# Kernel optimization log

Hardware: AMD Instinct MI355X
Metric: run time of the kernel (lower is better)

The kernel has to match this reference:

```python
import jax, jax.numpy as jnp
import numpy as np

B, S, V, D, H, L = 256, 512, 32000, 100, 75, 128

def setup_inputs() -> dict:
    key = jax.random.key(0)
    ks = jax.random.split(key, 10)
    def lin(k, out_f, in_f):
        bound = 1.0 / np.sqrt(in_f)
        kw, kb = jax.random.split(k)
        W = jax.random.uniform(kw, (out_f, in_f), jnp.float32, -bound, bound)
        b = jax.random.uniform(kb, (out_f,), jnp.float32, -bound, bound)
        return W, b
    W1, b1 = lin(ks[0], H, D)   # i2h_fc1
    W2, b2 = lin(ks[1], H, H)   # i2h_fc2
    Wo, bo = lin(ks[2], H, H)   # h2o_fc
    Wfc, bfc = lin(ks[3], L, H) # fc
    emb = jax.random.normal(ks[4], (V, D), jnp.float32)
    X = jax.random.randint(ks[5], (B, S), 0, V)
    return {"X": X, "emb": emb, "W1": W1, "b1": b1, "W2": W2, "b2": b2,
            "Wo": Wo, "bo": bo, "Wfc": Wfc, "bfc": bfc}

def reference(X, emb, W1, b1, W2, b2, Wo, bo, Wfc, bfc):
    x = emb[X]                                   # [B,S,D] embedding lookup (dropout off: is_training=False)
    xp = jnp.einsum('bsd,hd->bsh', x, W1) + b1   # precompute input projection for all steps
    h0 = jnp.zeros((X.shape[0], W2.shape[0]), x.dtype)

    def step(h, xp_t):
        h = jax.nn.sigmoid(xp_t + h @ W2.T + b2)       # Elman hidden update
        o = jax.nn.sigmoid(h @ Wo.T + bo)              # per-step output
        return h, o

    _, outs = jax.lax.scan(step, h0, jnp.swapaxes(xp, 0, 1))  # [S,B,H]
    outs = jnp.swapaxes(outs, 0, 1)                            # [B,S,H] (batch_first)
    return jnp.einsum('bsh,lh->bsl', outs, Wfc) + bfc          # [B,S,L]
```

## Files before the change

kernel.cpp:

```cpp
#include <hip/hip_runtime.h>
#include <hip/hip_bf16.h>

typedef unsigned int uint;
typedef unsigned short ushort;

constexpr int Bn = 256, Sn = 512, Vn = 32000, Dn = 100, Hn = 75, Ln = 128;
constexpr int EW = 80;
constexpr int KP = 96;
constexpr int W2S = 80;

constexpr size_t OFF_EMBW = 0;
constexpr size_t OFF_HALL = OFF_EMBW + (size_t)Vn*EW;
constexpr size_t OFF_W2P  = OFF_HALL + (size_t)Bn*Sn*KP/2;
constexpr size_t OFF_WOH  = OFF_W2P + 3200;
constexpr size_t OFF_WFH  = OFF_WOH + 3840;

typedef __attribute__((ext_vector_type(2))) _Float16 half2_t;
typedef __attribute__((ext_vector_type(8))) _Float16 half8;
typedef __attribute__((ext_vector_type(4))) float floatx4;

__device__ __forceinline__ ushort f2h(float f){
    union { _Float16 h; ushort u; } v; v.h = (_Float16)f; return v.u;
}
__device__ __forceinline__ half8 as_h8(uint4 u){
    union { uint4 u; half8 h; } v; v.u = u; return v.h;
}
__device__ __forceinline__ float sigmoidf(float z){
    return __builtin_amdgcn_rcpf(1.f + __expf(-z));
}

__global__ __launch_bounds__(256) void k_wprep(
    const float* __restrict__ W2, const float* __restrict__ Wo,
    const float* __restrict__ Wfc, ushort* __restrict__ w2p,
    ushort* __restrict__ woh, ushort* __restrict__ wfh, ushort* __restrict__ h_all)
{
    const int tid = blockIdx.x*256 + threadIdx.x;
    const int stride = gridDim.x*256;
    for (int i = tid; i < 80*W2S; i += stride){
        int r = i / W2S, k = i % W2S;
        w2p[i] = (r < Hn && k < Hn) ? f2h(W2[r*Hn + k]) : (ushort)0;
    }
    for (int i = tid; i < 80*KP; i += stride){
        int r = i / KP, k = i % KP;
        woh[i] = (r < Hn && k < Hn) ? f2h(Wo[r*Hn + k]) : (ushort)0;
    }
    for (int i = tid; i < Ln*KP; i += stride){
        int l = i / KP, k = i % KP;
        wfh[i] = (k < Hn) ? f2h(Wfc[l*Hn + k]) : (ushort)0;
    }
    uint* hu = (uint*)h_all;
    for (int i = tid; i < Bn*Sn*8; i += stride){
        int row = i >> 3, c = i & 7;
        hu[(size_t)row*48 + 40 + c] = 0u;
    }
}

__global__ __attribute__((amdgpu_flat_work_group_size(256,256)))
__attribute__((amdgpu_waves_per_eu(1,1)))
void k_embproj(
    const float* __restrict__ emb, const float* __restrict__ W1,
    const float* __restrict__ b1, const float* __restrict__ b2,
    float* __restrict__ embW)
{
    const int lane = threadIdx.x & 63;
    const int w    = threadIdx.x >> 6;
    const int v = blockIdx.x*64 + lane;
    const float4* ev = (const float4*)(emb + (size_t)v*Dn);
    float e[Dn];
    #pragma unroll
    for (int q = 0; q < Dn/4; ++q){
        float4 x = ev[q];
        e[4*q] = x.x; e[4*q+1] = x.y; e[4*q+2] = x.z; e[4*q+3] = x.w;
    }
    __shared__ float s_out[64*EW];
    const int j0 = w*19;
    const int jend = (w == 3) ? 18 : 19;
    #pragma unroll 2
    for (int jj = 0; jj < jend; ++jj){
        int j = j0 + jj;
        float a0 = b1[j] + b2[j], a1 = 0.f, a2 = 0.f, a3 = 0.f;
        const float* wp = W1 + j*Dn;
        #pragma unroll
        for (int d = 0; d < Dn; d += 4){
            a0 += wp[d]*e[d];     a1 += wp[d+1]*e[d+1];
            a2 += wp[d+2]*e[d+2]; a3 += wp[d+3]*e[d+3];
        }
        s_out[lane*EW + j] = (a0+a1) + (a2+a3);
    }
    if (w == 3){
        #pragma unroll
        for (int j = Hn; j < EW; ++j) s_out[lane*EW + j] = 0.f;
    }
    __syncthreads();
    float* dst = embW + (size_t)blockIdx.x*64*EW;
    for (int i = threadIdx.x; i < 64*EW; i += 256) dst[i] = s_out[i];
}

__global__ __attribute__((amdgpu_flat_work_group_size(256,256)))
__attribute__((amdgpu_waves_per_eu(1,1)))
void k_rnn(
    const int* __restrict__ X, const float* __restrict__ embW,
    const ushort* __restrict__ w2p, ushort* __restrict__ h_all,
    const ushort* __restrict__ woh, const ushort* __restrict__ wfh,
    const float* __restrict__ bo, const float* __restrict__ bfc,
    float* __restrict__ out)
{
    const int b   = blockIdx.x;
    const int tid = threadIdx.x;
    const int L   = tid & 63;
    const int wv  = tid >> 6;
    const int m   = L & 15;
    const int g   = L >> 4;
    __shared__ int sX[Sn];
    __shared__ __align__(16) float xpb[2][64*80];
    __shared__ __align__(16) ushort o_lds[4][16*104];

    for (int i = tid; i < Sn; i += 256) sX[i] = X[b*Sn + i];

    half8 bfr[5][3];
    if (wv == 0){
        #pragma unroll
        for (int t = 0; t < 5; ++t){
            #pragma unroll
            for (int ks = 0; ks < 3; ++ks){
                int k0 = ks*32 + g*8;
                half8 bv = {};
                if (k0 < 80) bv = *(const half8*)(w2p + (size_t)(16*t + m)*W2S + k0);
                bfr[t][ks] = bv;
            }
        }
    }
    __syncthreads();

    auto stage = [&](int c){
        float* buf = xpb[c & 1];
        const int base = c*64;
        #pragma unroll
        for (int k = 0; k < 5; ++k){
            int idx = k*256 + tid;
            int cs  = idx / 20;
            int off = idx - cs*20;
            int tok = sX[base + cs];
            const float* src = embW + (size_t)tok*EW + off*4;
            __builtin_amdgcn_global_load_lds(
                (const __attribute__((address_space(1))) uint*)src,
                (__attribute__((address_space(3))) uint*)(buf + idx*4),
                16, 0, 0);
        }
    };

    int va0 = 32*g,      va1 = 32*g + 8,  va2 = 32*g + 16, va3 = 32*g + 24;
    int vb0 = va0 + 128, vb1 = va1 + 128, vb2 = va2 + 128, vb3 = va3 + 128;

    ushort* hout = h_all + (size_t)b*Sn*KP;
    const floatx4 zero4 = {};
    uint4 A0 = {}, A1 = {}, A2 = {};

    stage(0);
    for (int c = 0; c < 8; ++c){
        __syncthreads();
        if (c < 7) stage(c + 1);
        if (wv == 0){
            const float* xp = xpb[c & 1];
            float x1c = xp[L];
            float x2c = (L < 16) ? xp[64 + L] : 0.f;
            float x1n = xp[80 + L];
            float x2n = (L < 16) ? xp[80 + 64 + L] : 0.f;
            for (int t = 0; t < 64; ++t){
                int pf = (t + 2 < 64) ? t + 2 : 63;
                float x1f = xp[pf*80 + L];
                float x2f = (L < 16) ? xp[pf*80 + 64 + L] : 0.f;

                half8 af0 = as_h8(A0), af1 = as_h8(A1), af2 = as_h8(A2);

                floatx4 acc0, acc1, acc2, acc3, acc4;
                acc0 = __builtin_amdgcn_mfma_f32_16x16x32_f16(af0, bfr[0][0], zero4, 0,0,0);
                acc1 = __builtin_amdgcn_mfma_f32_16x16x32_f16(af0, bfr[1][0], zero4, 0,0,0);
                acc2 = __builtin_amdgcn_mfma_f32_16x16x32_f16(af0, bfr[2][0], zero4, 0,0,0);
                acc3 = __builtin_amdgcn_mfma_f32_16x16x32_f16(af0, bfr[3][0], zero4, 0,0,0);
                acc4 = __builtin_amdgcn_mfma_f32_16x16x32_f16(af0, bfr[4][0], zero4, 0,0,0);
                acc0 = __builtin_amdgcn_mfma_f32_16x16x32_f16(af1, bfr[0][1], acc0, 0,0,0);
                acc1 = __builtin_amdgcn_mfma_f32_16x16x32_f16(af1, bfr[1][1], acc1, 0,0,0);
                acc2 = __builtin_amdgcn_mfma_f32_16x16x32_f16(af1, bfr[2][1], acc2, 0,0,0);
                acc3 = __builtin_amdgcn_mfma_f32_16x16x32_f16(af1, bfr[3][1], acc3, 0,0,0);
                acc4 = __builtin_amdgcn_mfma_f32_16x16x32_f16(af1, bfr[4][1], acc4, 0,0,0);
                acc0 = __builtin_amdgcn_mfma_f32_16x16x32_f16(af2, bfr[0][2], acc0, 0,0,0);
                acc1 = __builtin_amdgcn_mfma_f32_16x16x32_f16(af2, bfr[1][2], acc1, 0,0,0);
                acc2 = __builtin_amdgcn_mfma_f32_16x16x32_f16(af2, bfr[2][2], acc2, 0,0,0);
                acc3 = __builtin_amdgcn_mfma_f32_16x16x32_f16(af2, bfr[3][2], acc3, 0,0,0);
                acc4 = __builtin_amdgcn_mfma_f32_16x16x32_f16(af2, bfr[4][2], acc4, 0,0,0);

                float y1 = (L < 32) ? ((L < 16) ? acc0[0] : acc1[0])
                                    : ((L < 48) ? acc2[0] : acc3[0]);
                float y2 = acc4[0];

                float h1 = sigmoidf(y1 + x1c);
                float h2 = sigmoidf(y2 + x2c);
                if (L >= 11) h2 = 0.f;
                ushort u1 = f2h(h1);
                ushort u2 = f2h(h2);
                int s = c*64 + t;
                hout[(size_t)s*KP + L] = u1;
                if (L < 16) hout[(size_t)s*KP + 64 + L] = u2;

                uint v1 = u1, v2 = u2;
                uint pr1 = (uint)__builtin_amdgcn_update_dpp(0, (int)v1, 0xB1, 0xF, 0xF, true);
                uint pr2 = (uint)__builtin_amdgcn_update_dpp(0, (int)v2, 0xB1, 0xF, 0xF, true);
                int q1 = (int)(v1 | (pr1 << 16));
                int q2 = (int)(v2 | (pr2 << 16));

                A0.x = (uint)__builtin_amdgcn_ds_bpermute(va0, q1);
                A0.y = (uint)__builtin_amdgcn_ds_bpermute(va1, q1);
                A0.z = (uint)__builtin_amdgcn_ds_bpermute(va2, q1);
                A0.w = (uint)__builtin_amdgcn_ds_bpermute(va3, q1);
                A1.x = (uint)__builtin_amdgcn_ds_bpermute(vb0, q1);
                A1.y = (uint)__builtin_amdgcn_ds_bpermute(vb1, q1);
                A1.z = (uint)__builtin_amdgcn_ds_bpermute(vb2, q1);
                A1.w = (uint)__builtin_amdgcn_ds_bpermute(vb3, q1);
                A2.x = (uint)__builtin_amdgcn_ds_bpermute(va0, q2);
                A2.y = (uint)__builtin_amdgcn_ds_bpermute(va1, q2);
                A2.z = (uint)__builtin_amdgcn_ds_bpermute(va2, q2);
                A2.w = (uint)__builtin_amdgcn_ds_bpermute(va3, q2);

                x1c = x1n; x2c = x2n; x1n = x1f; x2n = x2f;
            }
        }
    }
    __syncthreads();

    ushort* ot = o_lds[wv];
    for (int i = L; i < 128; i += 64){
        int row = i >> 3, cw = i & 7;
        *(uint*)&ot[row*104 + 80 + cw*2] = 0u;
    }
    for (int it = 0; it < 8; ++it){
        const size_t r0 = (size_t)b*Sn + it*64 + wv*16;
        floatx4 acc1[5] = {};
        const ushort* hbase = h_all + r0*KP;
        #pragma unroll
        for (int ks = 0; ks < 3; ++ks){
            half8 a = *(const half8*)(hbase + (size_t)m*KP + ks*32 + g*8);
            #pragma unroll
            for (int t = 0; t < 5; ++t){
                half8 bt = *(const half8*)(woh + (16*t + m)*KP + ks*32 + g*8);
                acc1[t] = __builtin_amdgcn_mfma_f32_16x16x32_f16(a, bt, acc1[t], 0, 0, 0);
            }
        }
        #pragma unroll
        for (int t = 0; t < 5; ++t){
            int n = 16*t + m;
            float bias = (n < Hn) ? bo[n] : 0.f;
            #pragma unroll
            for (int r = 0; r < 4; ++r){
                int row = g*4 + r;
                float o = sigmoidf(acc1[t][r] + bias);
                if (n >= Hn) o = 0.f;
                ot[row*104 + n] = f2h(o);
            }
        }
        floatx4 acc2[8] = {};
        #pragma unroll
        for (int ks = 0; ks < 3; ++ks){
            half8 a = *(const half8*)(ot + m*104 + ks*32 + g*8);
            #pragma unroll
            for (int t = 0; t < 8; ++t){
                half8 bt = *(const half8*)(wfh + (16*t + m)*KP + ks*32 + g*8);
                acc2[t] = __builtin_amdgcn_mfma_f32_16x16x32_f16(a, bt, acc2[t], 0, 0, 0);
            }
        }
        float* orow = out + r0*Ln;
        #pragma unroll
        for (int t = 0; t < 8; ++t){
            float bias = bfc[16*t + m];
            #pragma unroll
            for (int r = 0; r < 4; ++r){
                int row = g*4 + r;
                orow[(size_t)row*Ln + 16*t + m] = acc2[t][r] + bias;
            }
        }
    }
}

extern "C" void kernel_launch(void* const* d_in, const int* in_sizes, int n_in,
                              void* d_out, int out_size, void* d_ws, size_t ws_size,
                              hipStream_t stream)
{
    const int*   X   = (const int*)d_in[0];
    const float* emb = (const float*)d_in[1];
    const float* W1  = (const float*)d_in[2];
    const float* b1  = (const float*)d_in[3];
    const float* W2  = (const float*)d_in[4];
    const float* b2  = (const float*)d_in[5];
    const float* Wo  = (const float*)d_in[6];
    const float* bo  = (const float*)d_in[7];
    const float* Wfc = (const float*)d_in[8];
    const float* bfc = (const float*)d_in[9];
    float* out = (float*)d_out;
    float* ws  = (float*)d_ws;

    float*  embW = ws + OFF_EMBW;
    ushort* hall = (ushort*)(ws + OFF_HALL);
    ushort* w2p  = (ushort*)(ws + OFF_W2P);
    ushort* woh  = (ushort*)(ws + OFF_WOH);
    ushort* wfh  = (ushort*)(ws + OFF_WFH);

    k_wprep<<<dim3(512), dim3(256), 0, stream>>>(W2, Wo, Wfc, w2p, woh, wfh, hall);
    k_embproj<<<dim3(Vn/64), dim3(256), 0, stream>>>(emb, W1, b1, b2, embW);
    k_rnn<<<dim3(Bn), dim3(256), 0, stream>>>(X, embW, w2p, hall, woh, wfh, bo, bfc, out);
}
```

Before: 316.6 us.

## Fuse input projection into RNN kernel and keep hidden states in LDS

The separate kernel that projected the whole 32000-row embedding table through W1 is removed. Instead, the three idle waves of each RNN block compute the projection on the fly for the next 64-step chunk of gathered tokens while wave 0 runs the recurrence. The full hidden-state history is now kept in LDS rather than written to and re-read from global memory, and the output stage reuses the xp buffer. This drops a large precompute pass and a global round trip, at the cost of redundant per-token projection work and a large LDS footprint per block.

```diff
diff --git a/kernel.cpp b/kernel.cpp
--- a/kernel.cpp
+++ b/kernel.cpp
@@ -5,15 +5,13 @@
 typedef unsigned short ushort;
 
 constexpr int Bn = 256, Sn = 512, Vn = 32000, Dn = 100, Hn = 75, Ln = 128;
-constexpr int EW = 80;
 constexpr int KP = 96;
 constexpr int W2S = 80;
-
-constexpr size_t OFF_EMBW = 0;
-constexpr size_t OFF_HALL = OFF_EMBW + (size_t)Vn*EW;
-constexpr size_t OFF_W2P  = OFF_HALL + (size_t)Bn*Sn*KP/2;
-constexpr size_t OFF_WOH  = OFF_W2P + 3200;
-constexpr size_t OFF_WFH  = OFF_WOH + 3840;
+constexpr int HS  = 104;
+
+constexpr size_t OFF_W2P = 0;
+constexpr size_t OFF_WOH = 3200;
+constexpr size_t OFF_WFH = OFF_WOH + 3840;
 
 typedef __attribute__((ext_vector_type(2))) _Float16 half2_t;
 typedef __attribute__((ext_vector_type(8))) _Float16 half8;
@@ -32,7 +30,7 @@
 __global__ __launch_bounds__(256) void k_wprep(
     const float* __restrict__ W2, const float* __restrict__ Wo,
     const float* __restrict__ Wfc, ushort* __restrict__ w2p,
-    ushort* __restrict__ woh, ushort* __restrict__ wfh, ushort* __restrict__ h_all)
+    ushort* __restrict__ woh, ushort* __restrict__ wfh)
 {
     const int tid = blockIdx.x*256 + threadIdx.x;
     const int stride = gridDim.x*256;
@@ -48,59 +46,14 @@
         int l = i / KP, k = i % KP;
         wfh[i] = (k < Hn) ? f2h(Wfc[l*Hn + k]) : (ushort)0;
     }
-    uint* hu = (uint*)h_all;
-    for (int i = tid; i < Bn*Sn*8; i += stride){
-        int row = i >> 3, c = i & 7;
-        hu[(size_t)row*48 + 40 + c] = 0u;
-    }
-}
-
-__global__ __attribute__((amdgpu_flat_work_group_size(256,256)))
-__attribute__((amdgpu_waves_per_eu(1,1)))
-void k_embproj(
-    const float* __restrict__ emb, const float* __restrict__ W1,
-    const float* __restrict__ b1, const float* __restrict__ b2,
-    float* __restrict__ embW)
-{
-    const int lane = threadIdx.x & 63;
-    const int w    = threadIdx.x >> 6;
-    const int v = blockIdx.x*64 + lane;
-    const float4* ev = (const float4*)(emb + (size_t)v*Dn);
-    float e[Dn];
-    #pragma unroll
-    for (int q = 0; q < Dn/4; ++q){
-        float4 x = ev[q];
-        e[4*q] = x.x; e[4*q+1] = x.y; e[4*q+2] = x.z; e[4*q+3] = x.w;
-    }
-    __shared__ float s_out[64*EW];
-    const int j0 = w*19;
-    const int jend = (w == 3) ? 18 : 19;
-    #pragma unroll 2
-    for (int jj = 0; jj < jend; ++jj){
-        int j = j0 + jj;
-        float a0 = b1[j] + b2[j], a1 = 0.f, a2 = 0.f, a3 = 0.f;
-        const float* wp = W1 + j*Dn;
-        #pragma unroll
-        for (int d = 0; d < Dn; d += 4){
-            a0 += wp[d]*e[d];     a1 += wp[d+1]*e[d+1];
-            a2 += wp[d+2]*e[d+2]; a3 += wp[d+3]*e[d+3];
-        }
-        s_out[lane*EW + j] = (a0+a1) + (a2+a3);
-    }
-    if (w == 3){
-        #pragma unroll
-        for (int j = Hn; j < EW; ++j) s_out[lane*EW + j] = 0.f;
-    }
-    __syncthreads();
-    float* dst = embW + (size_t)blockIdx.x*64*EW;
-    for (int i = threadIdx.x; i < 64*EW; i += 256) dst[i] = s_out[i];
 }
 
 __global__ __attribute__((amdgpu_flat_work_group_size(256,256)))
 __attribute__((amdgpu_waves_per_eu(1,1)))
 void k_rnn(
-    const int* __restrict__ X, const float* __restrict__ embW,
-    const ushort* __restrict__ w2p, ushort* __restrict__ h_all,
+    const int* __restrict__ X, const float* __restrict__ emb,
+    const float* __restrict__ W1, const float* __restrict__ b1,
+    const float* __restrict__ b2, const ushort* __restrict__ w2p,
     const ushort* __restrict__ woh, const ushort* __restrict__ wfh,
     const float* __restrict__ bo, const float* __restrict__ bfc,
     float* __restrict__ out)
@@ -113,9 +66,40 @@
     const int g   = L >> 4;
     __shared__ int sX[Sn];
     __shared__ __align__(16) float xpb[2][64*80];
-    __shared__ __align__(16) ushort o_lds[4][16*104];
+    __shared__ __align__(16) ushort hls[Sn*HS];
 
     for (int i = tid; i < Sn; i += 256) sX[i] = X[b*Sn + i];
+    for (int i = tid; i < Sn*8; i += 256){
+        int row = i >> 3, cw = i & 7;
+        ((uint*)hls)[row*(HS/2) + 40 + cw] = 0u;
+    }
+
+    const float bl1 = b1[L] + b2[L];
+    const float bl2 = (L < 11) ? (b1[64 + L] + b2[64 + L]) : 0.f;
+    const float4* wrow_a = (const float4*)(W1 + (size_t)L*Dn);
+    const int j2 = (64 + L < Hn) ? (64 + L) : (Hn - 1);
+    const float4* wrow_b = (const float4*)(W1 + (size_t)j2*Dn);
+
+    auto compute_xp = [&](int c, int lo, int hi){
+        float* buf = xpb[c & 1];
+        const int base = c*64;
+        for (int tt = lo; tt < hi; ++tt){
+            int tok = sX[base + tt];
+            const float4* er = (const float4*)(emb + (size_t)tok*Dn);
+            float a0 = bl1, a1 = 0.f, a2 = 0.f, a3 = 0.f;
+            float c0 = bl2, c1 = 0.f, c2 = 0.f, c3 = 0.f;
+            #pragma unroll
+            for (int d = 0; d < Dn/4; ++d){
+                float4 e4 = er[d], w4 = wrow_a[d], v4 = wrow_b[d];
+                a0 += w4.x*e4.x; a1 += w4.y*e4.y;
+                a2 += w4.z*e4.z; a3 += w4.w*e4.w;
+                c0 += v4.x*e4.x; c1 += v4.y*e4.y;
+                c2 += v4.z*e4.z; c3 += v4.w*e4.w;
+            }
+            buf[tt*80 + L] = (a0+a1) + (a2+a3);
+            if (L < 16) buf[tt*80 + 64 + L] = (L < 11) ? ((c0+c1)+(c2+c3)) : 0.f;
+        }
+    };
 
     half8 bfr[5][3];
     if (wv == 0){
@@ -132,35 +116,23 @@
     }
     __syncthreads();
 
-    auto stage = [&](int c){
-        float* buf = xpb[c & 1];
-        const int base = c*64;
-        #pragma unroll
-        for (int k = 0; k < 5; ++k){
-            int idx = k*256 + tid;
-            int cs  = idx / 20;
-            int off = idx - cs*20;
-            int tok = sX[base + cs];
-            const float* src = embW + (size_t)tok*EW + off*4;
-            __builtin_amdgcn_global_load_lds(
-                (const __attribute__((address_space(1))) uint*)src,
-                (__attribute__((address_space(3))) uint*)(buf + idx*4),
-                16, 0, 0);
-        }
-    };
+    compute_xp(0, wv*16, wv*16 + 16);
 
     int va0 = 32*g,      va1 = 32*g + 8,  va2 = 32*g + 16, va3 = 32*g + 24;
     int vb0 = va0 + 128, vb1 = va1 + 128, vb2 = va2 + 128, vb3 = va3 + 128;
 
-    ushort* hout = h_all + (size_t)b*Sn*KP;
     const floatx4 zero4 = {};
     uint4 A0 = {}, A1 = {}, A2 = {};
 
-    stage(0);
     for (int c = 0; c < 8; ++c){
         __syncthreads();
-        if (c < 7) stage(c + 1);
-        if (wv == 0){
+        if (wv != 0){
+            if (c < 7){
+                int lo = (wv == 1) ? 0  : (wv == 2) ? 22 : 43;
+                int hi = (wv == 1) ? 22 : (wv == 2) ? 43 : 64;
+                compute_xp(c + 1, lo, hi);
+            }
+        } else {
             const float* xp = xpb[c & 1];
             float x1c = xp[L];
             float x2c = (L < 16) ? xp[64 + L] : 0.f;
@@ -200,8 +172,8 @@
                 ushort u1 = f2h(h1);
                 ushort u2 = f2h(h2);
                 int s = c*64 + t;
-                hout[(size_t)s*KP + L] = u1;
-                if (L < 16) hout[(size_t)s*KP + 64 + L] = u2;
+                hls[(size_t)s*HS + L] = u1;
+                if (L < 16) hls[(size_t)s*HS + 64 + L] = u2;
 
                 uint v1 = u1, v2 = u2;
                 uint pr1 = (uint)__builtin_amdgcn_update_dpp(0, (int)v1, 0xB1, 0xF, 0xF, true);
@@ -228,18 +200,17 @@
     }
     __syncthreads();
 
-    ushort* ot = o_lds[wv];
+    ushort* ot = (ushort*)xpb + wv*(16*HS);
     for (int i = L; i < 128; i += 64){
         int row = i >> 3, cw = i & 7;
-        *(uint*)&ot[row*104 + 80 + cw*2] = 0u;
+        *(uint*)&ot[row*HS + 80 + cw*2] = 0u;
     }
     for (int it = 0; it < 8; ++it){
-        const size_t r0 = (size_t)b*Sn + it*64 + wv*16;
+        const int r0l = it*64 + wv*16;
         floatx4 acc1[5] = {};
-        const ushort* hbase = h_all + r0*KP;
         #pragma unroll
         for (int ks = 0; ks < 3; ++ks){
-            half8 a = *(const half8*)(hbase + (size_t)m*KP + ks*32 + g*8);
+            half8 a = *(const half8*)(hls + (size_t)(r0l + m)*HS + ks*32 + g*8);
             #pragma unroll
             for (int t = 0; t < 5; ++t){
                 half8 bt = *(const half8*)(woh + (16*t + m)*KP + ks*32 + g*8);
@@ -255,20 +226,20 @@
                 int row = g*4 + r;
                 float o = sigmoidf(acc1[t][r] + bias);
                 if (n >= Hn) o = 0.f;
-                ot[row*104 + n] = f2h(o);
+                ot[row*HS + n] = f2h(o);
             }
         }
         floatx4 acc2[8] = {};
         #pragma unroll
         for (int ks = 0; ks < 3; ++ks){
-            half8 a = *(const half8*)(ot + m*104 + ks*32 + g*8);
+            half8 a = *(const half8*)(ot + m*HS + ks*32 + g*8);
             #pragma unroll
             for (int t = 0; t < 8; ++t){
                 half8 bt = *(const half8*)(wfh + (16*t + m)*KP + ks*32 + g*8);
                 acc2[t] = __builtin_amdgcn_mfma_f32_16x16x32_f16(a, bt, acc2[t], 0, 0, 0);
             }
         }
-        float* orow = out + r0*Ln;
+        float* orow = out + ((size_t)b*Sn + r0l)*Ln;
         #pragma unroll
         for (int t = 0; t < 8; ++t){
             float bias = bfc[16*t + m];
@@ -298,13 +269,11 @@
     float* out = (float*)d_out;
     float* ws  = (float*)d_ws;
 
-    float*  embW = ws + OFF_EMBW;
-    ushort* hall = (ushort*)(ws + OFF_HALL);
-    ushort* w2p  = (ushort*)(ws + OFF_W2P);
-    ushort* woh  = (ushort*)(ws + OFF_WOH);
-    ushort* wfh  = (ushort*)(ws + OFF_WFH);
-
-    k_wprep<<<dim3(512), dim3(256), 0, stream>>>(W2, Wo, Wfc, w2p, woh, wfh, hall);
-    k_embproj<<<dim3(Vn/64), dim3(256), 0, stream>>>(emb, W1, b1, b2, embW);
-    k_rnn<<<dim3(Bn), dim3(256), 0, stream>>>(X, embW, w2p, hall, woh, wfh, bo, bfc, out);
-}
+    ushort* w2p = (ushort*)(ws + OFF_W2P);
+    ushort* woh = (ushort*)(ws + OFF_WOH);
+    ushort* wfh = (ushort*)(ws + OFF_WFH);
+
+    k_wprep<<<dim3(32), dim3(256), 0, stream>>>(W2, Wo, Wfc, w2p, woh, wfh);
+    k_rnn<<<dim3(Bn), dim3(256), 0, stream>>>(X, emb, W1, b1, b2, w2p,
+                                              woh, wfh, bo, bfc, out);
+}
```

New measurement: 931.8 us. +194.3%, slower.
